# Performance work log

Measured on AMD Instinct MI355X. Metric: run time of the kernel, lower is better.

The kernel has to match this reference:

```python
import jax, jax.numpy as jnp
import numpy as np

DIM = 128
HEADS = 8
C = DIM // HEADS  # per-head channel dim = 16
H = W = 256
B = 2


def setup_inputs() -> dict:
    key = jax.random.key(0)
    ks = jax.random.split(key, 6)
    x = jax.random.normal(ks[0], (B, DIM, H, W), jnp.float32)
    qkv_w = jax.random.normal(ks[1], (3 * DIM, DIM, 1, 1), jnp.float32) * 0.05
    dw_w = jax.random.normal(ks[2], (3 * DIM, 1, 3, 3), jnp.float32) * 0.05  # depthwise, groups=3*dim
    proj_w = jax.random.normal(ks[3], (DIM, DIM, 1, 1), jnp.float32) * 0.05
    attca_w = jax.random.normal(ks[4], (2 * C, C, 1, 1), jnp.float32) * 0.05
    temperature = jnp.ones((HEADS, 1, 1), jnp.float32)
    return {"x": x, "qkv_w": qkv_w, "dw_w": dw_w, "proj_w": proj_w,
            "attca_w": attca_w, "temperature": temperature}


def reference(x, qkv_w, dw_w, proj_w, attca_w, temperature):
    b, c_full, h, w = x.shape
    heads = temperature.shape[0]
    c = c_full // heads
    L = h * w

    # 1x1 conv qkv (pointwise -> einsum)
    qkv = jnp.einsum('bihw,oi->bohw', x, qkv_w[:, :, 0, 0])
    # 3x3 depthwise conv, groups = 3*dim
    qkv = jax.lax.conv_general_dilated(
        qkv, dw_w, window_strides=(1, 1), padding='SAME',
        dimension_numbers=('NCHW', 'OIHW', 'NCHW'),
        feature_group_count=3 * c_full)
    q, k, v = jnp.split(qkv, 3, axis=1)

    def to_heads(t):  # b (head c) h w -> b head c L
        return t.reshape(b, heads, c, L)
    q, k, v = to_heads(q), to_heads(k), to_heads(v)

    # F.normalize along last dim (eps=1e-12)
    q = q / jnp.maximum(jnp.linalg.norm(q, axis=-1, keepdims=True), 1e-12)
    k = k / jnp.maximum(jnp.linalg.norm(k, axis=-1, keepdims=True), 1e-12)

    # channel-wise attention scores: [b, head, c, c]
    attn = jnp.einsum('bhcl,bhdl->bhcd', q, k) * temperature

    attn0 = jax.nn.softmax(attn, axis=-1)
    a1 = jnp.square(jax.nn.relu(attn))
    a1 = jax.nn.gelu(a1, approximate=False) * a1

    # 'b head L c -> b c head L' then 1x1 conv over the (last) channel axis c
    a1p = jnp.transpose(a1, (0, 3, 1, 2))  # [b, c, head, c]
    xatt = jnp.einsum('bihd,oi->bohd', a1p, attca_w[:, :, 0, 0])  # [b, 2c, head, c]
    xatt = jnp.transpose(xatt, (0, 2, 3, 1))  # [b, head, c, 2c]
    scale, shift = jnp.split(xatt, 2, axis=-1)

    attn = attn0 * (1 + scale) + shift
    out = jnp.einsum('bhcd,bhdl->bhcl', attn, v).reshape(b, c_full, h, w)
    out = jnp.einsum('bihw,oi->bohw', out, proj_w[:, :, 0, 0])
    return out
```

## Files before the change

### kernel.cpp

```cpp
#include <hip/hip_runtime.h>
#include <hip/hip_bf16.h>
#include <math.h>

#define LL 65536
#define HH 256
#define WW 256
#define BB 2
#define DIMC 128
#define QKVC 384
#define NH 8
#define CH 16

typedef __hip_bfloat16 bf16;
typedef __attribute__((ext_vector_type(8))) __bf16 bf16x8;
typedef __attribute__((ext_vector_type(4))) float f32x4;
typedef __attribute__((ext_vector_type(4))) unsigned int u32x4;

static __device__ __forceinline__ float b2f(bf16 v){ return __bfloat162float(v); }
static __device__ __forceinline__ unsigned short fbits(float v){
  return __builtin_bit_cast(unsigned short, __float2bfloat16(v));
}
static __device__ __forceinline__ float us2f(unsigned short u){
  return __bfloat162float(__builtin_bit_cast(bf16, u));
}

__global__ void k_wb(const float* __restrict__ w, unsigned short* __restrict__ wb){
  int idx = blockIdx.x*256 + threadIdx.x;
  if (idx < QKVC*DIMC) wb[idx] = fbits(w[idx]);
}

__global__ __launch_bounds__(512) void k_pw(const float* __restrict__ x,
                                            const unsigned short* __restrict__ wb,
                                            unsigned short* __restrict__ qkv){
  __shared__ u32x4 lds4[2048];
  char* lds = (char*)lds4;
  unsigned short* lds16 = (unsigned short*)lds4;
  int bid = blockIdx.x;
  int b = bid >> 9;
  int l0 = (bid & 511) << 7;
  int tid = threadIdx.x;
  const float* xb = x + (size_t)b*DIMC*LL;

  #pragma unroll
  for (int it=0; it<4; ++it){
    int task = it*512 + tid;
    int l   = task & 127;
    int oct = task >> 7;
    float v[8];
    #pragma unroll
    for (int e=0;e<8;++e) v[e] = xb[(size_t)(oct*8+e)*LL + l0 + l];
    u32x4 p;
    #pragma unroll
    for (int k=0;k<4;++k){
      unsigned lo = fbits(v[2*k]);
      unsigned hi = fbits(v[2*k+1]);
      p[k] = lo | (hi<<16);
    }
    *(u32x4*)(lds + l*256 + ((oct ^ (l&15))<<4)) = p;
  }
  __syncthreads();

  int wid = tid >> 6, lane = tid & 63;
  int r = lane & 15, kg = lane >> 4;
  int ob = wid * 48;
  f32x4 acc[3][8];
  #pragma unroll
  for (int ft=0; ft<3; ++ft)
    #pragma unroll
    for (int nt=0; nt<8; ++nt) acc[ft][nt] = (f32x4)0.f;

  #pragma unroll
  for (int kb=0; kb<4; ++kb){
    bf16x8 a[3], bf[8];
    #pragma unroll
    for (int ft=0; ft<3; ++ft)
      a[ft] = *(const bf16x8*)(wb + (size_t)(ob + ft*16 + r)*DIMC + kb*32 + kg*8);
    #pragma unroll
    for (int nt=0; nt<8; ++nt){
      int l = nt*16 + r;
      bf[nt] = *(const bf16x8*)(lds + l*256 + (((kb*4 + kg) ^ r)<<4));
    }
    #pragma unroll
    for (int ft=0; ft<3; ++ft)
      #pragma unroll
      for (int nt=0; nt<8; ++nt)
        acc[ft][nt] = __builtin_amdgcn_mfma_f32_16x16x32_bf16(a[ft], bf[nt], acc[ft][nt], 0,0,0);
  }

  unsigned short* qb = qkv + (size_t)b*QKVC*LL + l0;
  int gl = tid & 15;
  int rowid = tid >> 4;
  #pragma unroll
  for (int ft=0; ft<3; ++ft){
    __syncthreads();
    #pragma unroll
    for (int nt=0; nt<8; ++nt)
      #pragma unroll
      for (int i=0;i<4;++i){
        int o_l = wid*16 + kg*4 + i;
        int l = nt*16 + r;
        lds16[o_l*128 + (((l>>3) ^ ((o_l>>1)&7))<<3) + (l&7)] = fbits(acc[ft][nt][i]);
      }
    __syncthreads();
    #pragma unroll
    for (int j=0;j<4;++j){
      int o_l = rowid*4 + j;
      u32x4 v = *(u32x4*)(lds16 + o_l*128 + ((gl ^ ((o_l>>1)&7))<<3));
      int o_g = (o_l>>4)*48 + ft*16 + (o_l&15);
      *(u32x4*)(qb + (size_t)o_g*LL + gl*8) = v;
    }
  }
}

__global__ __launch_bounds__(256) void k_dw(const unsigned short* __restrict__ src_,
                                            const float* __restrict__ dw,
                                            unsigned short* __restrict__ dst_){
  int bid = blockIdx.x;
  int band = bid & 31;
  int ch = (bid >> 5) % QKVC;
  int b  = bid / (QKVC*32);
  int t = threadIdx.x;
  int rowl = t >> 5;
  int seg  = t & 31;
  int grow = band*8 + rowl;
  const unsigned short* src = src_ + ((size_t)b*QKVC + ch)*LL;
  const float* w9 = dw + ch*9;

  float v[3][8];
  #pragma unroll
  for (int dy=0; dy<3; ++dy){
    int rr = grow + dy - 1;
    if (rr >= 0 && rr < HH){
      u32x4 raw = *(const u32x4*)(src + (size_t)rr*WW + seg*8);
      #pragma unroll
      for (int k=0;k<4;++k){
        v[dy][2*k]   = us2f((unsigned short)(raw[k] & 0xffffu));
        v[dy][2*k+1] = us2f((unsigned short)(raw[k] >> 16));
      }
    } else {
      #pragma unroll
      for (int e=0;e<8;++e) v[dy][e] = 0.f;
    }
  }
  int lane = t & 63;
  float lft[3], rgt[3];
  #pragma unroll
  for (int dy=0; dy<3; ++dy){
    float lv = __shfl(v[dy][7], lane-1);
    float rv = __shfl(v[dy][0], lane+1);
    lft[dy] = (seg==0)  ? 0.f : lv;
    rgt[dy] = (seg==31) ? 0.f : rv;
  }
  float w0=w9[0],w1=w9[1],w2=w9[2],w3=w9[3],w4=w9[4],w5=w9[5],w6=w9[6],w7=w9[7],w8=w9[8];
  float o[8];
  #pragma unroll
  for (int e=0;e<8;++e){
    float l0 = (e==0) ? lft[0] : v[0][e-1];
    float l1 = (e==0) ? lft[1] : v[1][e-1];
    float l2 = (e==0) ? lft[2] : v[2][e-1];
    float r0 = (e==7) ? rgt[0] : v[0][e+1];
    float r1 = (e==7) ? rgt[1] : v[1][e+1];
    float r2 = (e==7) ? rgt[2] : v[2][e+1];
    float a;
    a = w0*l0;            a = fmaf(w1, v[0][e], a); a = fmaf(w2, r0, a);
    a = fmaf(w3, l1, a);  a = fmaf(w4, v[1][e], a); a = fmaf(w5, r1, a);
    a = fmaf(w6, l2, a);  a = fmaf(w7, v[2][e], a); a = fmaf(w8, r2, a);
    o[e] = a;
  }
  u32x4 pk;
  #pragma unroll
  for (int k=0;k<4;++k){
    unsigned lo = fbits(o[2*k]);
    unsigned hi = fbits(o[2*k+1]);
    pk[k] = lo | (hi<<16);
  }
  *(u32x4*)(dst_ + ((size_t)b*QKVC + ch)*LL + (size_t)grow*WW + seg*8) = pk;
}

__global__ __launch_bounds__(256) void k_gram(const unsigned short* __restrict__ qkvd,
                                              float* __restrict__ S,
                                              float* __restrict__ nq,
                                              float* __restrict__ nk){
  int bid = blockIdx.x;
  int chunk = bid & 63;
  int h = (bid>>6)&7;
  int b = bid>>9;
  int tid = threadIdx.x, wid = tid>>6, lane = tid&63;
  int r = lane&15, kg = lane>>4;
  int l0 = chunk*1024 + wid*256;
  const unsigned short* qb = qkvd + (size_t)(b*QKVC + h*CH)*LL;
  const unsigned short* kb = qkvd + (size_t)(b*QKVC + DIMC + h*CH)*LL;
  f32x4 sqk = (f32x4)0.f, sqq = (f32x4)0.f, skk = (f32x4)0.f;
  #pragma unroll 4
  for (int ks=0; ks<8; ++ks){
    int l = l0 + ks*32 + kg*8;
    bf16x8 qf = *(const bf16x8*)(qb + (size_t)r*LL + l);
    bf16x8 kf = *(const bf16x8*)(kb + (size_t)r*LL + l);
    sqk = __builtin_amdgcn_mfma_f32_16x16x32_bf16(qf, kf, sqk, 0,0,0);
    sqq = __builtin_amdgcn_mfma_f32_16x16x32_bf16(qf, qf, sqq, 0,0,0);
    skk = __builtin_amdgcn_mfma_f32_16x16x32_bf16(kf, kf, skk, 0,0,0);
  }
  float* Sb = S + (size_t)((b*NH + h)*CH)*CH;
  #pragma unroll
  for (int i=0;i<4;++i)
    atomicAdd(&Sb[(kg*4+i)*CH + r], sqk[i]);
  if ((r>>2) == kg){
    int i = r&3;
    atomicAdd(&nq[(b*NH+h)*CH + r], sqq[i]);
    atomicAdd(&nk[(b*NH+h)*CH + r], skk[i]);
  }
}

__global__ __launch_bounds__(256) void k_fin(const float* __restrict__ S,
                                             const float* __restrict__ nq,
                                             const float* __restrict__ nk,
                                             const float* __restrict__ temp,
                                             const float* __restrict__ attca,
                                             const float* __restrict__ proj,
                                             unsigned short* __restrict__ M2){
  int b = blockIdx.x;
  int t = threadIdx.x;
  __shared__ float attnf[NH][CH][CH];
  __shared__ float pl[DIMC*DIMC];
  for (int idx=t; idx<DIMC*DIMC; idx+=256) pl[idx] = proj[idx];
  if (t < 128){
    int h = t >> 4, c = t & 15;
    float tmpv = temp[h];
    float qn = fmaxf(sqrtf(nq[(b*NH+h)*CH + c]), 1e-12f);
    float row[CH], ex[CH], a1[CH];
    float m = -1e30f;
    #pragma unroll
    for (int d=0; d<CH; ++d){
      float kn = fmaxf(sqrtf(nk[(b*NH+h)*CH + d]), 1e-12f);
      float v = S[((b*NH+h)*CH + c)*CH + d] / (qn*kn) * tmpv;
      row[d] = v;
      m = fmaxf(m, v);
    }
    float sum = 0.f;
    #pragma unroll
    for (int d=0;d<CH;++d){ ex[d] = expf(row[d]-m); sum += ex[d]; }
    float inv = 1.f/sum;
    #pragma unroll
    for (int d=0;d<CH;++d){
      float rr = fmaxf(row[d], 0.f);
      float xx = rr*rr;
      float g = 0.5f * xx * (1.f + erff(xx * 0.70710678118654752440f));
      a1[d] = g * xx;
    }
    #pragma unroll
    for (int j=0;j<CH;++j){
      float sc=0.f, sh=0.f;
      #pragma unroll
      for (int i=0;i<CH;++i){
        sc = fmaf(attca[j*CH+i],      a1[i], sc);
        sh = fmaf(attca[(CH+j)*CH+i], a1[i], sh);
      }
      attnf[h][c][j] = ex[j]*inv*(1.f+sc) + sh;
    }
  }
  __syncthreads();
  for (int idx=t; idx<DIMC*DIMC; idx+=256){
    int o = idx >> 7, j = idx & 127;
    int h = j >> 4, d = j & 15;
    float s = 0.f;
    #pragma unroll
    for (int c2=0;c2<CH;++c2) s = fmaf(pl[o*DIMC + h*CH + c2], attnf[h][c2][d], s);
    M2[(size_t)b*DIMC*DIMC + o*DIMC + j] = fbits(s);
  }
}

__global__ __launch_bounds__(256) void k_out(const unsigned short* __restrict__ qkvd,
                                             const unsigned short* __restrict__ M2,
                                             float* __restrict__ out){
  __shared__ u32x4 lds4[2048];
  char* lds = (char*)lds4;
  int bid = blockIdx.x;
  int b = bid >> 9;
  int l0 = (bid & 511) << 7;
  int tid = threadIdx.x;
  const unsigned short* vb = qkvd + (size_t)(b*QKVC + 2*DIMC)*LL;

  #pragma unroll
  for (int it=0; it<4; ++it){
    int task = it*256 + tid;
    int lp  = (task & 63) * 2;
    int oct = task >> 6;
    unsigned lo32[8];
    #pragma unroll
    for (int e=0;e<8;++e)
      lo32[e] = *(const unsigned int*)(vb + (size_t)(oct*8+e)*LL + l0 + lp);
    u32x4 p0, p1;
    #pragma unroll
    for (int k=0;k<4;++k){
      unsigned a0 = lo32[2*k] & 0xffffu,  a1 = lo32[2*k] >> 16;
      unsigned b0 = lo32[2*k+1] & 0xffffu, b1 = lo32[2*k+1] >> 16;
      p0[k] = a0 | (b0<<16);
      p1[k] = a1 | (b1<<16);
    }
    *(u32x4*)(lds + lp*256     + ((oct ^ (lp&15))<<4))     = p0;
    *(u32x4*)(lds + (lp+1)*256 + ((oct ^ ((lp+1)&15))<<4)) = p1;
  }
  __syncthreads();

  int wid = tid >> 6, lane = tid & 63;
  int r = lane & 15, kg = lane >> 4;
  int ob = wid * 32;
  f32x4 acc[2][8];
  #pragma unroll
  for (int ft=0; ft<2; ++ft)
    #pragma unroll
    for (int nt=0; nt<8; ++nt) acc[ft][nt] = (f32x4)0.f;

  #pragma unroll
  for (int kb=0; kb<4; ++kb){
    bf16x8 a[2], bf[8];
    #pragma unroll
    for (int ft=0; ft<2; ++ft)
      a[ft] = *(const bf16x8*)(M2 + (size_t)b*DIMC*DIMC + (ob + ft*16 + r)*DIMC + kb*32 + kg*8);
    #pragma unroll
    for (int nt=0; nt<8; ++nt){
      int l = nt*16 + r;
      bf[nt] = *(const bf16x8*)(lds + l*256 + (((kb*4 + kg) ^ r)<<4));
    }
    #pragma unroll
    for (int ft=0; ft<2; ++ft)
      #pragma unroll
      for (int nt=0; nt<8; ++nt)
        acc[ft][nt] = __builtin_amdgcn_mfma_f32_16x16x32_bf16(a[ft], bf[nt], acc[ft][nt], 0,0,0);
  }

  float* ob_ptr = out + (size_t)b*DIMC*LL + l0;
  #pragma unroll
  for (int ft=0; ft<2; ++ft)
    #pragma unroll
    for (int nt=0; nt<8; ++nt)
      #pragma unroll
      for (int i=0;i<4;++i){
        int o = ob + ft*16 + kg*4 + i;
        ob_ptr[(size_t)o*LL + nt*16 + r] = acc[ft][nt][i];
      }
}

extern "C" void kernel_launch(void* const* d_in, const int* in_sizes, int n_in,
                              void* d_out, int out_size, void* d_ws, size_t ws_size,
                              hipStream_t stream){
  const float* x      = (const float*)d_in[0];
  const float* qkv_w  = (const float*)d_in[1];
  const float* dw_w   = (const float*)d_in[2];
  const float* proj_w = (const float*)d_in[3];
  const float* attca  = (const float*)d_in[4];
  const float* temp   = (const float*)d_in[5];
  float* out = (float*)d_out;

  char* ws = (char*)d_ws;
  size_t off = 0;
  unsigned short* qkv_pw = (unsigned short*)(ws + off); off += (size_t)BB*QKVC*LL*2;
  unsigned short* qkv_dw = (unsigned short*)(ws + off); off += (size_t)BB*QKVC*LL*2;
  float* S  = (float*)(ws + off); off += (size_t)BB*NH*CH*CH*4;
  float* nq = (float*)(ws + off); off += (size_t)BB*NH*CH*4;
  float* nk = (float*)(ws + off); off += (size_t)BB*NH*CH*4;
  unsigned short* wb = (unsigned short*)(ws + off); off += (size_t)QKVC*DIMC*2;
  unsigned short* M2 = (unsigned short*)(ws + off); off += (size_t)BB*DIMC*DIMC*2;

  hipMemsetAsync(S, 0, (size_t)(BB*NH*CH*CH + 2*BB*NH*CH)*4, stream);

  k_wb  <<<(QKVC*DIMC + 255)/256, 256, 0, stream>>>(qkv_w, wb);
  k_pw  <<<BB*512,       512, 0, stream>>>(x, wb, qkv_pw);
  k_dw  <<<BB*QKVC*32,   256, 0, stream>>>(qkv_pw, dw_w, qkv_dw);
  k_gram<<<BB*512,       256, 0, stream>>>(qkv_dw, S, nq, nk);
  k_fin <<<BB,           256, 0, stream>>>(S, nq, nk, temp, attca, proj_w, M2);
  k_out <<<BB*512,       256, 0, stream>>>(qkv_dw, M2, out);
}
```

Measured before the change: 254.7 us.

## Shrink spatial tiles in pointwise and output GEMM kernels for more blocks

The qkv pointwise kernel now uses 256-thread blocks over 32-pixel tiles (4x more blocks), with each wave computing 96 output channels. It drops the LDS-staged, 16-byte-vectorized store epilogue in favour of direct 2-byte scattered global stores. The output projection kernel halves its tile to 64 pixels, doubling the block count. The aim is more parallelism and occupancy, at the cost of less weight reuse per block and narrower, less coalesced stores in the pointwise kernel.

```diff
diff --git a/kernel.cpp b/kernel.cpp
--- a/kernel.cpp
+++ b/kernel.cpp
@@ -16,7 +16,6 @@
 typedef __attribute__((ext_vector_type(4))) float f32x4;
 typedef __attribute__((ext_vector_type(4))) unsigned int u32x4;
 
-static __device__ __forceinline__ float b2f(bf16 v){ return __bfloat162float(v); }
 static __device__ __forceinline__ unsigned short fbits(float v){
   return __builtin_bit_cast(unsigned short, __float2bfloat16(v));
 }
@@ -29,23 +28,22 @@
   if (idx < QKVC*DIMC) wb[idx] = fbits(w[idx]);
 }
 
-__global__ __launch_bounds__(512) void k_pw(const float* __restrict__ x,
+__global__ __launch_bounds__(256) void k_pw(const float* __restrict__ x,
                                             const unsigned short* __restrict__ wb,
                                             unsigned short* __restrict__ qkv){
-  __shared__ u32x4 lds4[2048];
+  __shared__ u32x4 lds4[512];
   char* lds = (char*)lds4;
-  unsigned short* lds16 = (unsigned short*)lds4;
   int bid = blockIdx.x;
-  int b = bid >> 9;
-  int l0 = (bid & 511) << 7;
+  int b = bid >> 11;
+  int l0 = (bid & 2047) << 5;
   int tid = threadIdx.x;
   const float* xb = x + (size_t)b*DIMC*LL;
 
   #pragma unroll
-  for (int it=0; it<4; ++it){
-    int task = it*512 + tid;
-    int l   = task & 127;
-    int oct = task >> 7;
+  for (int it=0; it<2; ++it){
+    int task = it*256 + tid;
+    int l   = task & 31;
+    int oct = task >> 5;
     float v[8];
     #pragma unroll
     for (int e=0;e<8;++e) v[e] = xb[(size_t)(oct*8+e)*LL + l0 + l];
@@ -62,54 +60,40 @@
 
   int wid = tid >> 6, lane = tid & 63;
   int r = lane & 15, kg = lane >> 4;
-  int ob = wid * 48;
-  f32x4 acc[3][8];
-  #pragma unroll
-  for (int ft=0; ft<3; ++ft)
-    #pragma unroll
-    for (int nt=0; nt<8; ++nt) acc[ft][nt] = (f32x4)0.f;
+  int ob = wid * 96;
+  f32x4 acc[6][2];
+  #pragma unroll
+  for (int ft=0; ft<6; ++ft)
+    #pragma unroll
+    for (int nt=0; nt<2; ++nt) acc[ft][nt] = (f32x4)0.f;
 
   #pragma unroll
   for (int kb=0; kb<4; ++kb){
-    bf16x8 a[3], bf[8];
-    #pragma unroll
-    for (int ft=0; ft<3; ++ft)
-      a[ft] = *(const bf16x8*)(wb + (size_t)(ob + ft*16 + r)*DIMC + kb*32 + kg*8);
-    #pragma unroll
-    for (int nt=0; nt<8; ++nt){
+    bf16x8 bfv[2];
+    #pragma unroll
+    for (int nt=0; nt<2; ++nt){
       int l = nt*16 + r;
-      bf[nt] = *(const bf16x8*)(lds + l*256 + (((kb*4 + kg) ^ r)<<4));
-    }
-    #pragma unroll
-    for (int ft=0; ft<3; ++ft)
-      #pragma unroll
-      for (int nt=0; nt<8; ++nt)
-        acc[ft][nt] = __builtin_amdgcn_mfma_f32_16x16x32_bf16(a[ft], bf[nt], acc[ft][nt], 0,0,0);
+      bfv[nt] = *(const bf16x8*)(lds + l*256 + (((kb*4 + kg) ^ r)<<4));
+    }
+    #pragma unroll
+    for (int ft=0; ft<6; ++ft){
+      bf16x8 a = *(const bf16x8*)(wb + (size_t)(ob + ft*16 + r)*DIMC + kb*32 + kg*8);
+      #pragma unroll
+      for (int nt=0; nt<2; ++nt)
+        acc[ft][nt] = __builtin_amdgcn_mfma_f32_16x16x32_bf16(a, bfv[nt], acc[ft][nt], 0,0,0);
+    }
   }
 
   unsigned short* qb = qkv + (size_t)b*QKVC*LL + l0;
-  int gl = tid & 15;
-  int rowid = tid >> 4;
-  #pragma unroll
-  for (int ft=0; ft<3; ++ft){
-    __syncthreads();
-    #pragma unroll
-    for (int nt=0; nt<8; ++nt)
+  #pragma unroll
+  for (int ft=0; ft<6; ++ft)
+    #pragma unroll
+    for (int nt=0; nt<2; ++nt)
       #pragma unroll
       for (int i=0;i<4;++i){
-        int o_l = wid*16 + kg*4 + i;
-        int l = nt*16 + r;
-        lds16[o_l*128 + (((l>>3) ^ ((o_l>>1)&7))<<3) + (l&7)] = fbits(acc[ft][nt][i]);
+        int o = ob + ft*16 + kg*4 + i;
+        qb[(size_t)o*LL + nt*16 + r] = fbits(acc[ft][nt][i]);
       }
-    __syncthreads();
-    #pragma unroll
-    for (int j=0;j<4;++j){
-      int o_l = rowid*4 + j;
-      u32x4 v = *(u32x4*)(lds16 + o_l*128 + ((gl ^ ((o_l>>1)&7))<<3));
-      int o_g = (o_l>>4)*48 + ft*16 + (o_l&15);
-      *(u32x4*)(qb + (size_t)o_g*LL + gl*8) = v;
-    }
-  }
 }
 
 __global__ __launch_bounds__(256) void k_dw(const unsigned short* __restrict__ src_,
@@ -272,19 +256,19 @@
 __global__ __launch_bounds__(256) void k_out(const unsigned short* __restrict__ qkvd,
                                              const unsigned short* __restrict__ M2,
                                              float* __restrict__ out){
-  __shared__ u32x4 lds4[2048];
+  __shared__ u32x4 lds4[1024];
   char* lds = (char*)lds4;
   int bid = blockIdx.x;
-  int b = bid >> 9;
-  int l0 = (bid & 511) << 7;
+  int b = bid >> 10;
+  int l0 = (bid & 1023) << 6;
   int tid = threadIdx.x;
   const unsigned short* vb = qkvd + (size_t)(b*QKVC + 2*DIMC)*LL;
 
   #pragma unroll
-  for (int it=0; it<4; ++it){
+  for (int it=0; it<2; ++it){
     int task = it*256 + tid;
-    int lp  = (task & 63) * 2;
-    int oct = task >> 6;
+    int lp  = (task & 31) * 2;
+    int oct = task >> 5;
     unsigned lo32[8];
     #pragma unroll
     for (int e=0;e<8;++e)
@@ -305,35 +289,34 @@
   int wid = tid >> 6, lane = tid & 63;
   int r = lane & 15, kg = lane >> 4;
   int ob = wid * 32;
-  f32x4 acc[2][8];
+  f32x4 acc[2][4];
   #pragma unroll
   for (int ft=0; ft<2; ++ft)
     #pragma unroll
-    for (int nt=0; nt<8; ++nt) acc[ft][nt] = (f32x4)0.f;
+    for (int nt=0; nt<4; ++nt) acc[ft][nt] = (f32x4)0.f;
 
   #pragma unroll
   for (int kb=0; kb<4; ++kb){
-    bf16x8 a[2], bf[8];
-    #pragma unroll
-    for (int ft=0; ft<2; ++ft)
-      a[ft] = *(const bf16x8*)(M2 + (size_t)b*DIMC*DIMC + (ob + ft*16 + r)*DIMC + kb*32 + kg*8);
-    #pragma unroll
-    for (int nt=0; nt<8; ++nt){
+    bf16x8 bfv[4];
+    #pragma unroll
+    for (int nt=0; nt<4; ++nt){
       int l = nt*16 + r;
-      bf[nt] = *(const bf16x8*)(lds + l*256 + (((kb*4 + kg) ^ r)<<4));
-    }
-    #pragma unroll
-    for (int ft=0; ft<2; ++ft)
-      #pragma unroll
-      for (int nt=0; nt<8; ++nt)
-        acc[ft][nt] = __builtin_amdgcn_mfma_f32_16x16x32_bf16(a[ft], bf[nt], acc[ft][nt], 0,0,0);
+      bfv[nt] = *(const bf16x8*)(lds + l*256 + (((kb*4 + kg) ^ r)<<4));
+    }
+    #pragma unroll
+    for (int ft=0; ft<2; ++ft){
+      bf16x8 a = *(const bf16x8*)(M2 + (size_t)b*DIMC*DIMC + (ob + ft*16 + r)*DIMC + kb*32 + kg*8);
+      #pragma unroll
+      for (int nt=0; nt<4; ++nt)
+        acc[ft][nt] = __builtin_amdgcn_mfma_f32_16x16x32_bf16(a, bfv[nt], acc[ft][nt], 0,0,0);
+    }
   }
 
   float* ob_ptr = out + (size_t)b*DIMC*LL + l0;
   #pragma unroll
   for (int ft=0; ft<2; ++ft)
     #pragma unroll
-    for (int nt=0; nt<8; ++nt)
+    for (int nt=0; nt<4; ++nt)
       #pragma unroll
       for (int i=0;i<4;++i){
         int o = ob + ft*16 + kg*4 + i;
@@ -365,9 +348,9 @@
   hipMemsetAsync(S, 0, (size_t)(BB*NH*CH*CH + 2*BB*NH*CH)*4, stream);
 
   k_wb  <<<(QKVC*DIMC + 255)/256, 256, 0, stream>>>(qkv_w, wb);
-  k_pw  <<<BB*512,       512, 0, stream>>>(x, wb, qkv_pw);
+  k_pw  <<<BB*2048,      256, 0, stream>>>(x, wb, qkv_pw);
   k_dw  <<<BB*QKVC*32,   256, 0, stream>>>(qkv_pw, dw_w, qkv_dw);
   k_gram<<<BB*512,       256, 0, stream>>>(qkv_dw, S, nq, nk);
   k_fin <<<BB,           256, 0, stream>>>(S, nq, nk, temp, attca, proj_w, M2);
-  k_out <<<BB*512,       256, 0, stream>>>(qkv_dw, M2, out);
-}
+  k_out <<<BB*1024,      256, 0, stream>>>(qkv_dw, M2, out);
+}
```

Result: slower. 299.8 us (+17.7%).
